# Performance work log

Hardware: AMD Instinct MI355X
Metric: run time of the kernel (lower is better)

The kernel has to match this reference:

```python
import jax, jax.numpy as jnp
import numpy as np

LAYERS, HIDDEN, FFN, HEADS = 2, 128, 256, 4
IMG_H, IMG_W = 32, 64
SEQ = IMG_H * IMG_W
HEAD = HIDDEN // HEADS          # 32, per-head qk dim
HEAD_V = 2 * HEAD               # double_v_dim=True
VDIM = HEADS * HEAD_V           # 256
B = 2
SCALE_BASE = 512.0
EPS = 1e-5


def _xpos_tables(seq, d):
    # XPOS: rotary angles + per-position exponential scale
    half = d // 2
    scale_vec = (jnp.arange(0, d, 2, dtype=jnp.float32) + 0.4 * d) / (1.4 * d)  # (d/2,)
    power = jnp.arange(seq, dtype=jnp.float32) / SCALE_BASE
    scale = scale_vec[None, :] ** power[:, None]                                 # (S, d/2)
    inv_freq = 1.0 / (10000.0 ** (jnp.arange(half, dtype=jnp.float32) / half))
    ang = jnp.arange(seq, dtype=jnp.float32)[:, None] * inv_freq[None, :]        # (S, d/2)
    return jnp.sin(ang), jnp.cos(ang), scale


def _apply_xpos(x, sin, cos, scale):
    # duplicate-interleave sin/cos*scale to width d, rotate-every-two
    s = jnp.repeat(sin * scale, 2, axis=-1)   # (S, d)
    c = jnp.repeat(cos * scale, 2, axis=-1)
    x1, x2 = x[..., ::2], x[..., 1::2]
    rot = jnp.stack([-x2, x1], axis=-1).reshape(x.shape)
    return x * c + rot * s


def _ln(x, g, b):
    mu = x.mean(-1, keepdims=True)
    var = ((x - mu) ** 2).mean(-1, keepdims=True)
    return (x - mu) * jax.lax.rsqrt(var + EPS) * g + b


def _gn(y, g, b):
    # GroupNorm(HEADS groups) over VDIM channels, applied per token
    bsz, s, v = y.shape
    yg = y.reshape(bsz, s, HEADS, HEAD_V)
    mu = yg.mean(-1, keepdims=True)
    var = ((yg - mu) ** 2).mean(-1, keepdims=True)
    yn = ((yg - mu) * jax.lax.rsqrt(var + EPS)).reshape(bsz, s, v)
    return yn * g + b


def _decay(seq):
    # D[h, n, m] = gamma_h^(n-m) for n >= m else 0
    gammas = 1.0 - jnp.exp(jnp.linspace(jnp.log(1.0 / 32.0), jnp.log(1.0 / 512.0), HEADS))
    n = jnp.arange(seq, dtype=jnp.float32)
    diff = n[:, None] - n[None, :]
    return (gammas[:, None, None] ** jnp.maximum(diff, 0.0)) * (diff >= 0.0)


def _forward(x, ln1_g, ln1_b, ln2_g, ln2_b, WQ, WK, WV, WG, WO, gn_g, gn_b, w1, b1, w2, b2):
    sin, cos, scale = _xpos_tables(SEQ, HEAD)
    D = _decay(SEQ)  # (H, S, S)
    for i in range(LAYERS):
        h = _ln(x, ln1_g[i], ln1_b[i])
        Q = _apply_xpos(jnp.einsum('bsd,hde->bhse', h, WQ[i]), sin, cos, scale)
        K = _apply_xpos(jnp.einsum('bsd,hde->bhse', h, WK[i]), sin, cos, 1.0 / scale)
        V = jnp.einsum('bsd,hdv->bhsv', h, WV[i])
        att = jnp.einsum('bhse,bhte->bhst', Q, K) * D[None]      # decay retention
        Y = jnp.einsum('bhst,bhtv->bhsv', att, V)
        Y = jnp.moveaxis(Y, 1, 2).reshape(x.shape[0], SEQ, VDIM)  # concat heads
        Y = _gn(Y, gn_g[i], gn_b[i])
        G = h @ WG[i]
        ret = (G * jax.nn.sigmoid(G) * Y) @ WO[i]                 # swish gate + out proj
        y = ret + x
        h2 = _ln(y, ln2_g[i], ln2_b[i])
        x = jax.nn.gelu(h2 @ w1[i] + b1[i], approximate=False) @ w2[i] + b2[i] + y
    return x.reshape(x.shape[0], IMG_H, IMG_W, x.shape[-1])


def setup_inputs() -> dict:
    key = jax.random.key(0)
    ks = jax.random.split(key, 8)
    def rn(k, shape, sc):
        return jax.random.normal(k, shape, dtype=jnp.float32) * sc
    s = 1.0 / np.sqrt(HIDDEN)
    return {
        'x': rn(ks[0], (B, SEQ, HIDDEN), 1.0),
        'ln1_g': jnp.ones((LAYERS, HIDDEN), jnp.float32),
        'ln1_b': jnp.zeros((LAYERS, HIDDEN), jnp.float32),
        'ln2_g': jnp.ones((LAYERS, HIDDEN), jnp.float32),
        'ln2_b': jnp.zeros((LAYERS, HIDDEN), jnp.float32),
        'WQ': rn(ks[1], (LAYERS, HEADS, HIDDEN, HEAD), s),
        'WK': rn(ks[2], (LAYERS, HEADS, HIDDEN, HEAD), s),
        'WV': rn(ks[3], (LAYERS, HEADS, HIDDEN, HEAD_V), s),
        'WG': rn(ks[4], (LAYERS, HIDDEN, VDIM), s),
        'WO': rn(ks[5], (LAYERS, VDIM, HIDDEN), 1.0 / np.sqrt(VDIM)),
        'gn_g': jnp.ones((LAYERS, VDIM), jnp.float32),
        'gn_b': jnp.zeros((LAYERS, VDIM), jnp.float32),
        'w1': rn(ks[6], (LAYERS, HIDDEN, FFN), s),
        'b1': jnp.zeros((LAYERS, FFN), jnp.float32),
        'w2': rn(ks[7], (LAYERS, FFN, HIDDEN), 1.0 / np.sqrt(FFN)),
        'b2': jnp.zeros((LAYERS, HIDDEN), jnp.float32),
    }


def reference(x, ln1_g, ln1_b, ln2_g, ln2_b, WQ, WK, WV, WG, WO, gn_g, gn_b, w1, b1, w2, b2):
    return _forward(x, ln1_g, ln1_b, ln2_g, ln2_b, WQ, WK, WV, WG, WO, gn_g, gn_b, w1, b1, w2, b2)
```

## Files before the change

kernel.cpp:

```cpp
#include <hip/hip_runtime.h>
#include <math.h>

#define NLAYERS 2
#define HID 128
#define FFND 256
#define NH 4
#define SEQL 2048
#define HD 32
#define HDV 64
#define VD 256
#define NBATCH 2
#define MROWS (NBATCH*SEQL)
#define NCAT 768
#define NCHUNK 32

__global__ __launch_bounds__(256) void setup_kernel(
    const float* __restrict__ WQ, const float* __restrict__ WK,
    const float* __restrict__ WV, const float* __restrict__ WG,
    float* __restrict__ Wcat, float* __restrict__ tabs)
{
  int bid = blockIdx.x;
  if (bid < 768) {
    int idx = bid * 256 + threadIdx.x;
    int l = idx / (HID * NCAT);
    int r = idx - l * (HID * NCAT);
    int k = r / NCAT;
    int n = r - k * NCAT;
    float v;
    if (n < 128)      { int h = n >> 5, e = n & 31;            v = WQ[(((l*NH+h)*HID)+k)*HD  + e]; }
    else if (n < 256) { int m = n-128; int h = m>>5, e = m&31; v = WK[(((l*NH+h)*HID)+k)*HD  + e]; }
    else if (n < 512) { int m = n-256; int h = m>>6, e = m&63; v = WV[(((l*NH+h)*HID)+k)*HDV + e]; }
    else              { v = WG[(l*HID + k)*VD + (n-512)]; }
    Wcat[idx] = v;
  } else {
    int idx = (bid - 768) * 256 + threadIdx.x;
    int s = idx >> 4, i = idx & 15;
    float inv_freq = powf(10000.f, -(float)i * (1.f/16.f));
    float ang = (float)s * inv_freq;
    float sv  = ((float)(2*i) + 0.4f*32.f) / (1.4f*32.f);
    float sc  = powf(sv, (float)s * (1.f/512.f));
    float sn = sinf(ang), cs = cosf(ang);
    tabs[idx]          = sn * sc;
    tabs[32768 + idx]  = cs * sc;
    tabs[65536 + idx]  = sn / sc;
    tabs[98304 + idx]  = cs / sc;
  }
}

template<int CN, bool XPOS, bool BIAS, bool GELU>
__global__ __launch_bounds__(256) void gemm_ln(
    const float* __restrict__ A, const float* __restrict__ Bw,
    const float* __restrict__ lng, const float* __restrict__ lnb,
    const float* __restrict__ bias, const float* __restrict__ tabs,
    float* __restrict__ C, int N)
{
  constexpr int TN = 16 * CN;
  constexpr int BK = (CN == 8) ? 32 : 64;
  __shared__ float As[128][68];
  __shared__ float Bs[BK][TN + 4];

  int tid = threadIdx.x;
  int tx = tid & 15, ty = tid >> 4;
  int rb = blockIdx.x * 64, nb = blockIdx.y * TN;

  {
    int row = tid >> 2, q = tid & 3;
    const float* ar = A + (size_t)(rb + row) * HID + 32 * q;
    float4 av[8];
    #pragma unroll
    for (int it = 0; it < 8; it++) av[it] = *(const float4*)(ar + 4*it);
    float s = 0.f;
    #pragma unroll
    for (int it = 0; it < 8; it++) s += av[it].x + av[it].y + av[it].z + av[it].w;
    s += __shfl_xor(s, 1); s += __shfl_xor(s, 2);
    float mu = s * (1.f/128.f);
    float qs = 0.f;
    #pragma unroll
    for (int it = 0; it < 8; it++) {
      float d;
      d = av[it].x - mu; qs += d*d;  d = av[it].y - mu; qs += d*d;
      d = av[it].z - mu; qs += d*d;  d = av[it].w - mu; qs += d*d;
    }
    qs += __shfl_xor(qs, 1); qs += __shfl_xor(qs, 2);
    float rs = rsqrtf(qs * (1.f/128.f) + 1e-5f);
    int rsw = row ^ (16 * q);
    #pragma unroll
    for (int it = 0; it < 8; it++) {
      int k0 = 32*q + 4*it;
      float4 g4 = *(const float4*)(lng + k0);
      float4 b4 = *(const float4*)(lnb + k0);
      As[k0+0][rsw] = (av[it].x-mu)*rs*g4.x + b4.x;
      As[k0+1][rsw] = (av[it].y-mu)*rs*g4.y + b4.y;
      As[k0+2][rsw] = (av[it].z-mu)*rs*g4.z + b4.z;
      As[k0+3][rsw] = (av[it].w-mu)*rs*g4.w + b4.w;
    }
  }

  float acc[4][CN];
  #pragma unroll
  for (int i=0;i<4;i++)
    #pragma unroll
    for (int j=0;j<CN;j++) acc[i][j] = 0.f;

  for (int ks = 0; ks < 128; ks += BK) {
    #pragma unroll
    for (int it = 0; it < 4; it++) {
      int idx = it*256 + tid;
      int kk = idx / (TN/4), nq = idx % (TN/4);
      *(float4*)(&Bs[kk][4*nq]) =
          *(const float4*)(Bw + (size_t)(ks+kk)*N + nb + 4*nq);
    }
    __syncthreads();
    #pragma unroll
    for (int kk = 0; kk < BK; kk++) {
      int k = ks + kk;
      float a[4];
      *(float4*)a = *(const float4*)&As[k][(4*ty) ^ (16*(k>>5))];
      float b[CN];
      #pragma unroll
      for (int j4 = 0; j4 < CN; j4 += 4)
        *(float4*)(b+j4) = *(const float4*)&Bs[kk][CN*tx + j4];
      #pragma unroll
      for (int i=0;i<4;i++)
        #pragma unroll
        for (int j=0;j<CN;j++)
          acc[i][j] = fmaf(a[i], b[j], acc[i][j]);
    }
    __syncthreads();
  }

  #pragma unroll
  for (int i=0;i<4;i++) {
    int row = rb + 4*ty + i;
    int cb = nb + CN*tx;
    float o[CN];
    #pragma unroll
    for (int j=0;j<CN;j++) {
      float v = acc[i][j];
      if (BIAS)  v += bias[cb + j];
      if (GELU)  v = 0.5f * v * (1.f + erff(v * 0.70710678118f));
      o[j] = v;
    }
    if (XPOS) {
      if (nb < 256) {
        bool isK = (nb >= 128);
        const float* sn_t = tabs + (isK ? 65536 : 0);
        const float* cs_t = tabs + (isK ? 98304 : 32768);
        int s = row & (SEQL - 1);
        #pragma unroll
        for (int p = 0; p < CN/2; p++) {
          int i0 = ((cb + 2*p) & 31) >> 1;
          float sn = sn_t[s*16 + i0], cs = cs_t[s*16 + i0];
          float x1 = o[2*p], x2 = o[2*p+1];
          o[2*p]   = x1*cs - x2*sn;
          o[2*p+1] = x2*cs + x1*sn;
        }
      }
    }
    #pragma unroll
    for (int j4 = 0; j4 < CN; j4 += 4)
      *(float4*)(C + (size_t)row*N + cb + j4) = *(float4*)(o + j4);
  }
}

template<bool BIAS>
__global__ __launch_bounds__(256) void gemm_nar(
    const float* __restrict__ A, const float* __restrict__ Bw,
    const float* __restrict__ bias, const float* __restrict__ Rsd,
    float* __restrict__ C, int N)
{
  __shared__ float As[64][68];
  __shared__ float Bs[64][36];
  int tid = threadIdx.x;
  int tx = tid & 15, ty = tid >> 4;
  int rb = blockIdx.x * 64, nb = blockIdx.y * 32;

  float acc[4][2];
  #pragma unroll
  for (int i=0;i<4;i++) { acc[i][0]=0.f; acc[i][1]=0.f; }

  for (int ks = 0; ks < 256; ks += 64) {
    #pragma unroll
    for (int it = 0; it < 4; it++) {
      int idx = it*256 + tid;
      int row = idx >> 4, kq = idx & 15;
      float4 a4 = *(const float4*)(A + (size_t)(rb+row)*256 + ks + 4*kq);
      int rsw = row ^ (4*(kq & 7));
      As[4*kq+0][rsw] = a4.x; As[4*kq+1][rsw] = a4.y;
      As[4*kq+2][rsw] = a4.z; As[4*kq+3][rsw] = a4.w;
    }
    #pragma unroll
    for (int it = 0; it < 2; it++) {
      int idx = it*256 + tid;
      int kk = idx >> 3, nq = idx & 7;
      *(float4*)(&Bs[kk][4*nq]) =
          *(const float4*)(Bw + (size_t)(ks+kk)*N + nb + 4*nq);
    }
    __syncthreads();
    #pragma unroll
    for (int kk = 0; kk < 64; kk++) {
      float a[4];
      *(float4*)a = *(const float4*)&As[kk][(4*ty) ^ (4*((kk>>2)&7))];
      float2 b2 = *(const float2*)&Bs[kk][2*tx];
      #pragma unroll
      for (int i=0;i<4;i++) {
        acc[i][0] = fmaf(a[i], b2.x, acc[i][0]);
        acc[i][1] = fmaf(a[i], b2.y, acc[i][1]);
      }
    }
    __syncthreads();
  }

  #pragma unroll
  for (int i=0;i<4;i++) {
    int row = rb + 4*ty + i;
    int cb = nb + 2*tx;
    float o[2];
    #pragma unroll
    for (int j=0;j<2;j++) {
      float v = acc[i][j];
      if (BIAS) v += bias[cb + j];
      v += Rsd[(size_t)row*N + cb + j];
      o[j] = v;
    }
    *(float2*)(C + (size_t)row*N + cb) = *(float2*)o;
  }
}

__global__ __launch_bounds__(512) void ret_kv_kernel(
    const float* __restrict__ QKVG, float* __restrict__ Asum)
{
  int bh = blockIdx.x >> 5;
  int c  = blockIdx.x & 31;
  int b = bh >> 2, h = bh & 3;
  float t0 = logf(1.f/32.f) + (float)h * (logf(1.f/512.f) - logf(1.f/32.f)) * (1.f/3.f);
  float gamma = 1.f - expf(t0);
  float lg = logf(gamma);

  __shared__ float Ks[64][36];
  __shared__ float Vs[64][68];
  __shared__ float wt[64];

  int tid = threadIdx.x;
  int c0 = c * 64;
  const float* base = QKVG + (size_t)(b * SEQL) * NCAT;

  {
    int row = tid >> 3, eq = tid & 7;
    *(float4*)&Ks[row][4*eq] =
        *(const float4*)(base + (size_t)(c0+row)*NCAT + 128 + h*32 + 4*eq);
  }
  #pragma unroll
  for (int it = 0; it < 2; it++) {
    int idx = it*512 + tid;
    int row = idx >> 4, vq = idx & 15;
    *(float4*)&Vs[row][4*vq] =
        *(const float4*)(base + (size_t)(c0+row)*NCAT + 256 + h*64 + 4*vq);
  }
  if (tid < 64) wt[tid] = __expf(lg * (float)(64 - tid));
  __syncthreads();

  int e = tid >> 4, v4 = (tid & 15) * 4;
  float a0[4] = {0,0,0,0};
  #pragma unroll 8
  for (int t = 0; t < 64; t++) {
    float kw = Ks[t][e] * wt[t];
    float4 v0 = *(const float4*)&Vs[t][v4];
    a0[0] = fmaf(kw, v0.x, a0[0]); a0[1] = fmaf(kw, v0.y, a0[1]);
    a0[2] = fmaf(kw, v0.z, a0[2]); a0[3] = fmaf(kw, v0.w, a0[3]);
  }
  *(float4*)(Asum + ((size_t)(bh*NCHUNK + c))*2048 + e*64 + v4) = *(float4*)a0;
}

__global__ __launch_bounds__(512) void ret_out_kernel(
    const float* __restrict__ QKVG, const float* __restrict__ Asum,
    const float* __restrict__ gn_g, const float* __restrict__ gn_b,
    float* __restrict__ Gated)
{
  int bh = blockIdx.x >> 5;
  int c  = blockIdx.x & 31;
  int b = bh >> 2, h = bh & 3;
  float t0 = logf(1.f/32.f) + (float)h * (logf(1.f/512.f) - logf(1.f/32.f)) * (1.f/3.f);
  float gamma = 1.f - expf(t0);
  float lg = logf(gamma);
  float g64 = __expf(lg * 64.f);

  __shared__ float Qs[64][36];
  __shared__ float Ks[64][36];
  __shared__ float Vs[64][68];
  __shared__ float Ss[64][68];
  __shared__ float Sc[32][68];

  int tid = threadIdx.x;
  int tx2 = tid & 31, ty2 = tid >> 5;
  int c0 = c * 64;
  const float* base = QKVG + (size_t)(b * SEQL) * NCAT;

  {
    int row = tid >> 3, eq = tid & 7;
    *(float4*)&Qs[row][4*eq] =
        *(const float4*)(base + (size_t)(c0+row)*NCAT + h*32 + 4*eq);
    int esw = (4*eq) ^ (4*((row >> 2) & 7));
    *(float4*)&Ks[row][esw] =
        *(const float4*)(base + (size_t)(c0+row)*NCAT + 128 + h*32 + 4*eq);
  }
  #pragma unroll
  for (int it = 0; it < 2; it++) {
    int idx = it*512 + tid;
    int row = idx >> 4, vq = idx & 15;
    *(float4*)&Vs[row][4*vq] =
        *(const float4*)(base + (size_t)(c0+row)*NCAT + 256 + h*64 + 4*vq);
  }

  {
    int e = tid >> 4, v4 = (tid & 15) * 4;
    float s0[4] = {0,0,0,0};
    float w = 1.f;
    const float* ab = Asum + ((size_t)bh*NCHUNK)*2048 + e*64 + v4;
    for (int cp = c-1; cp >= 0; --cp) {
      const float* ap = ab + (size_t)cp*2048;
      float4 x0 = *(const float4*)ap;
      s0[0] = fmaf(w, x0.x, s0[0]); s0[1] = fmaf(w, x0.y, s0[1]);
      s0[2] = fmaf(w, x0.z, s0[2]); s0[3] = fmaf(w, x0.w, s0[3]);
      w *= g64;
    }
    *(float4*)&Sc[e][v4] = *(float4*)s0;
  }
  __syncthreads();

  float sacc[4][2];
  #pragma unroll
  for (int i=0;i<4;i++) { sacc[i][0]=0.f; sacc[i][1]=0.f; }
  #pragma unroll
  for (int e = 0; e < 32; e += 4) {
    float qv[4][4], kv[2][4];
    #pragma unroll
    for (int i=0;i<4;i++)
      *(float4*)qv[i] = *(const float4*)&Qs[4*ty2+i][e];
    #pragma unroll
    for (int j=0;j<2;j++) {
      int kr = 2*tx2 + j;
      *(float4*)kv[j] = *(const float4*)&Ks[kr][e ^ (4*((kr>>2)&7))];
    }
    #pragma unroll
    for (int i=0;i<4;i++)
      #pragma unroll
      for (int j=0;j<2;j++)
        sacc[i][j] = fmaf(qv[i][0], kv[j][0],
                     fmaf(qv[i][1], kv[j][1],
                     fmaf(qv[i][2], kv[j][2],
                     fmaf(qv[i][3], kv[j][3], sacc[i][j]))));
  }
  #pragma unroll
  for (int i=0;i<4;i++) {
    int sl = 4*ty2 + i;
    float o2[2];
    #pragma unroll
    for (int j=0;j<2;j++) {
      int dr = sl - (2*tx2 + j);
      float w = (dr >= 0) ? __expf(lg * (float)dr) : 0.f;
      o2[j] = sacc[i][j] * w;
    }
    *(float2*)&Ss[sl][2*tx2] = *(float2*)o2;
  }

  float acc[4][2];
  #pragma unroll
  for (int i=0;i<4;i++) { acc[i][0]=0.f; acc[i][1]=0.f; }
  #pragma unroll
  for (int e = 0; e < 32; e += 4) {
    float qv[4][4], sv[4][2];
    #pragma unroll
    for (int i=0;i<4;i++)
      *(float4*)qv[i] = *(const float4*)&Qs[4*ty2+i][e];
    #pragma unroll
    for (int m=0;m<4;m++)
      *(float2*)sv[m] = *(const float2*)&Sc[e+m][2*tx2];
    #pragma unroll
    for (int i=0;i<4;i++)
      #pragma unroll
      for (int j=0;j<2;j++)
        acc[i][j] = fmaf(qv[i][0], sv[0][j],
                    fmaf(qv[i][1], sv[1][j],
                    fmaf(qv[i][2], sv[2][j],
                    fmaf(qv[i][3], sv[3][j], acc[i][j]))));
  }
  #pragma unroll
  for (int i=0;i<4;i++) {
    float gr = __expf(lg * (float)(4*ty2 + i));
    acc[i][0] *= gr; acc[i][1] *= gr;
  }
  __syncthreads();

  #pragma unroll
  for (int t = 0; t < 64; t += 4) {
    float sv[4][4], vv[4][2];
    #pragma unroll
    for (int i=0;i<4;i++)
      *(float4*)sv[i] = *(const float4*)&Ss[4*ty2+i][t];
    #pragma unroll
    for (int m=0;m<4;m++)
      *(float2*)vv[m] = *(const float2*)&Vs[t+m][2*tx2];
    #pragma unroll
    for (int i=0;i<4;i++)
      #pragma unroll
      for (int j=0;j<2;j++)
        acc[i][j] = fmaf(sv[i][0], vv[0][j],
                    fmaf(sv[i][1], vv[1][j],
                    fmaf(sv[i][2], vv[2][j],
                    fmaf(sv[i][3], vv[3][j], acc[i][j]))));
  }

  #pragma unroll
  for (int i=0;i<4;i++) {
    float s1 = acc[i][0] + acc[i][1];
    #pragma unroll
    for (int o = 16; o; o >>= 1) s1 += __shfl_xor(s1, o);
    float mu = s1 * (1.f/64.f);
    float q = 0.f;
    #pragma unroll
    for (int j=0;j<2;j++) { float d = acc[i][j] - mu; q += d*d; }
    #pragma unroll
    for (int o = 16; o; o >>= 1) q += __shfl_xor(q, o);
    float rs = rsqrtf(q * (1.f/64.f) + 1e-5f);
    int row = b*SEQL + c0 + 4*ty2 + i;
    float2 g2 = *(const float2*)(QKVG + (size_t)row*NCAT + 512 + h*64 + 2*tx2);
    float gv[2] = {g2.x, g2.y};
    float o2[2];
    #pragma unroll
    for (int j=0;j<2;j++) {
      int col = h*64 + 2*tx2 + j;
      float yn = (acc[i][j] - mu) * rs * gn_g[col] + gn_b[col];
      float g = gv[j];
      float sig = 1.f / (1.f + __expf(-g));
      o2[j] = g * sig * yn;
    }
    *(float2*)(Gated + (size_t)row*VD + h*64 + 2*tx2) = *(float2*)o2;
  }
}

extern "C" void kernel_launch(void* const* d_in, const int* in_sizes, int n_in,
                              void* d_out, int out_size, void* d_ws, size_t ws_size,
                              hipStream_t stream)
{
  (void)in_sizes; (void)n_in; (void)out_size; (void)ws_size;
  const float* x_in  = (const float*)d_in[0];
  const float* ln1_g = (const float*)d_in[1];
  const float* ln1_b = (const float*)d_in[2];
  const float* ln2_g = (const float*)d_in[3];
  const float* ln2_b = (const float*)d_in[4];
  const float* WQ    = (const float*)d_in[5];
  const float* WK    = (const float*)d_in[6];
  const float* WV    = (const float*)d_in[7];
  const float* WG    = (const float*)d_in[8];
  const float* WO    = (const float*)d_in[9];
  const float* gn_g  = (const float*)d_in[10];
  const float* gn_b  = (const float*)d_in[11];
  const float* w1    = (const float*)d_in[12];
  const float* b1    = (const float*)d_in[13];
  const float* w2    = (const float*)d_in[14];
  const float* b2    = (const float*)d_in[15];
  float* out = (float*)d_out;
  float* ws  = (float*)d_ws;

  float* Wcat = ws;
  float* tabs = Wcat + 196608;
  float* QKVG = tabs + 131072;
  float* Asum = QKVG + 3145728;
  float* Gt   = Asum + 524288;
  float* Yres = Gt   + 1048576;
  float* Mid  = Yres + 524288;

  setup_kernel<<<896, 256, 0, stream>>>(WQ, WK, WV, WG, Wcat, tabs);

  for (int l = 0; l < NLAYERS; l++) {
    const float* xl = (l == 0) ? x_in : out;
    gemm_ln<8,true,false,false><<<dim3(MROWS/64, NCAT/128), 256, 0, stream>>>(
        xl, Wcat + l*HID*NCAT, ln1_g + l*HID, ln1_b + l*HID,
        nullptr, tabs, QKVG, NCAT);
    ret_kv_kernel<<<256, 512, 0, stream>>>(QKVG, Asum);
    ret_out_kernel<<<256, 512, 0, stream>>>(QKVG, Asum, gn_g + l*VD, gn_b + l*VD, Gt);
    gemm_nar<false><<<dim3(MROWS/64, HID/32), 256, 0, stream>>>(
        Gt, WO + l*VD*HID, nullptr, xl, Yres, HID);
    gemm_ln<4,false,true,true><<<dim3(MROWS/64, FFND/64), 256, 0, stream>>>(
        Yres, w1 + l*HID*FFND, ln2_g + l*HID, ln2_b + l*HID,
        b1 + l*FFND, nullptr, Mid, FFND);
    gemm_nar<true><<<dim3(MROWS/64, HID/32), 256, 0, stream>>>(
        Mid, w2 + l*FFND*HID, b2 + l*HID, Yres, out, HID);
  }
}
```

Measured before the change: 236.5 us.

## Fuse output projection, LayerNorm and FFN into one chained kernel

Replaces the three separate post-retention GEMM launches (WO plus residual, LN2+FFN1+GELU, FFN2 plus residual) with one ffn_chain kernel. It keeps each 16-row tile's intermediates in shared memory, so Yres and Mid no longer round-trip through global memory. The QKVG projection is split into a standalone LayerNorm kernel plus a new register-prefetched GEMM that computes the XPOS sin/cos/scale inline, which removes the precomputed tables. In exchange, each fused block re-streams all FFN weights for only 16 rows, and the projection epilogue now evaluates transcendentals per element.

```diff
diff --git a/kernel.cpp b/kernel.cpp
--- a/kernel.cpp
+++ b/kernel.cpp
@@ -14,216 +14,140 @@
 #define NCAT 768
 #define NCHUNK 32
 
-__global__ __launch_bounds__(256) void setup_kernel(
+#define LG32   (-3.4657359028f)
+#define DLT    (-0.9241962407f)
+__device__ __forceinline__ float lgamma_h(int h) {
+  return logf(1.f - expf(LG32 + DLT * (float)h));
+}
+
+__global__ __launch_bounds__(256) void pack_w_kernel(
     const float* __restrict__ WQ, const float* __restrict__ WK,
     const float* __restrict__ WV, const float* __restrict__ WG,
-    float* __restrict__ Wcat, float* __restrict__ tabs)
+    float* __restrict__ Wcat)
 {
-  int bid = blockIdx.x;
-  if (bid < 768) {
-    int idx = bid * 256 + threadIdx.x;
-    int l = idx / (HID * NCAT);
-    int r = idx - l * (HID * NCAT);
-    int k = r / NCAT;
-    int n = r - k * NCAT;
-    float v;
-    if (n < 128)      { int h = n >> 5, e = n & 31;            v = WQ[(((l*NH+h)*HID)+k)*HD  + e]; }
-    else if (n < 256) { int m = n-128; int h = m>>5, e = m&31; v = WK[(((l*NH+h)*HID)+k)*HD  + e]; }
-    else if (n < 512) { int m = n-256; int h = m>>6, e = m&63; v = WV[(((l*NH+h)*HID)+k)*HDV + e]; }
-    else              { v = WG[(l*HID + k)*VD + (n-512)]; }
-    Wcat[idx] = v;
-  } else {
-    int idx = (bid - 768) * 256 + threadIdx.x;
-    int s = idx >> 4, i = idx & 15;
-    float inv_freq = powf(10000.f, -(float)i * (1.f/16.f));
-    float ang = (float)s * inv_freq;
-    float sv  = ((float)(2*i) + 0.4f*32.f) / (1.4f*32.f);
-    float sc  = powf(sv, (float)s * (1.f/512.f));
-    float sn = sinf(ang), cs = cosf(ang);
-    tabs[idx]          = sn * sc;
-    tabs[32768 + idx]  = cs * sc;
-    tabs[65536 + idx]  = sn / sc;
-    tabs[98304 + idx]  = cs / sc;
-  }
-}
-
-template<int CN, bool XPOS, bool BIAS, bool GELU>
-__global__ __launch_bounds__(256) void gemm_ln(
-    const float* __restrict__ A, const float* __restrict__ Bw,
-    const float* __restrict__ lng, const float* __restrict__ lnb,
-    const float* __restrict__ bias, const float* __restrict__ tabs,
-    float* __restrict__ C, int N)
+  int idx = blockIdx.x * 256 + threadIdx.x;
+  if (idx >= NLAYERS * HID * NCAT) return;
+  int l = idx / (HID * NCAT);
+  int r = idx - l * (HID * NCAT);
+  int k = r / NCAT;
+  int n = r - k * NCAT;
+  float v;
+  if (n < 128)      { int h = n >> 5, e = n & 31;            v = WQ[(((l*NH+h)*HID)+k)*HD  + e]; }
+  else if (n < 256) { int m = n-128; int h = m>>5, e = m&31; v = WK[(((l*NH+h)*HID)+k)*HD  + e]; }
+  else if (n < 512) { int m = n-256; int h = m>>6, e = m&63; v = WV[(((l*NH+h)*HID)+k)*HDV + e]; }
+  else              { v = WG[(l*HID + k)*VD + (n-512)]; }
+  Wcat[idx] = v;
+}
+
+__global__ __launch_bounds__(256) void ln_rows_kernel(
+    const float* __restrict__ X, const float* __restrict__ g,
+    const float* __restrict__ b, float* __restrict__ O)
 {
-  constexpr int TN = 16 * CN;
-  constexpr int BK = (CN == 8) ? 32 : 64;
-  __shared__ float As[128][68];
-  __shared__ float Bs[BK][TN + 4];
-
+  int wid = threadIdx.x >> 6, lane = threadIdx.x & 63;
+  int row = blockIdx.x * 4 + wid;
+  const float* x = X + (size_t)row * HID;
+  float v0 = x[lane], v1 = x[lane + 64];
+  float s = v0 + v1;
+  #pragma unroll
+  for (int o = 32; o; o >>= 1) s += __shfl_xor(s, o);
+  float mu = s * (1.f/128.f);
+  float d0 = v0 - mu, d1 = v1 - mu;
+  float q = d0*d0 + d1*d1;
+  #pragma unroll
+  for (int o = 32; o; o >>= 1) q += __shfl_xor(q, o);
+  float rs = rsqrtf(q * (1.f/128.f) + 1e-5f);
+  O[(size_t)row*HID + lane]      = d0 * rs * g[lane]      + b[lane];
+  O[(size_t)row*HID + lane + 64] = d1 * rs * g[lane + 64] + b[lane + 64];
+}
+
+__global__ __launch_bounds__(512) void gemm_qkvg(
+    const float* __restrict__ H, const float* __restrict__ Wcat,
+    float* __restrict__ C)
+{
+  __shared__ float Bs[16][260];
   int tid = threadIdx.x;
-  int tx = tid & 15, ty = tid >> 4;
-  int rb = blockIdx.x * 64, nb = blockIdx.y * TN;
-
-  {
-    int row = tid >> 2, q = tid & 3;
-    const float* ar = A + (size_t)(rb + row) * HID + 32 * q;
-    float4 av[8];
-    #pragma unroll
-    for (int it = 0; it < 8; it++) av[it] = *(const float4*)(ar + 4*it);
-    float s = 0.f;
-    #pragma unroll
-    for (int it = 0; it < 8; it++) s += av[it].x + av[it].y + av[it].z + av[it].w;
-    s += __shfl_xor(s, 1); s += __shfl_xor(s, 2);
-    float mu = s * (1.f/128.f);
-    float qs = 0.f;
-    #pragma unroll
-    for (int it = 0; it < 8; it++) {
-      float d;
-      d = av[it].x - mu; qs += d*d;  d = av[it].y - mu; qs += d*d;
-      d = av[it].z - mu; qs += d*d;  d = av[it].w - mu; qs += d*d;
-    }
-    qs += __shfl_xor(qs, 1); qs += __shfl_xor(qs, 2);
-    float rs = rsqrtf(qs * (1.f/128.f) + 1e-5f);
-    int rsw = row ^ (16 * q);
-    #pragma unroll
-    for (int it = 0; it < 8; it++) {
-      int k0 = 32*q + 4*it;
-      float4 g4 = *(const float4*)(lng + k0);
-      float4 b4 = *(const float4*)(lnb + k0);
-      As[k0+0][rsw] = (av[it].x-mu)*rs*g4.x + b4.x;
-      As[k0+1][rsw] = (av[it].y-mu)*rs*g4.y + b4.y;
-      As[k0+2][rsw] = (av[it].z-mu)*rs*g4.z + b4.z;
-      As[k0+3][rsw] = (av[it].w-mu)*rs*g4.w + b4.w;
-    }
-  }
-
-  float acc[4][CN];
+  int tx = tid & 63, ty = tid >> 6;
+  int rb = blockIdx.x * 32, nb = blockIdx.y * 256;
+
+  float4 pre[2];
+  #pragma unroll
+  for (int it = 0; it < 2; it++) {
+    int f = it*512 + tid;
+    int kk = f >> 6, c4 = f & 63;
+    pre[it] = *(const float4*)(Wcat + (size_t)kk*NCAT + nb + 4*c4);
+  }
+
+  float acc[4][4];
   #pragma unroll
   for (int i=0;i<4;i++)
     #pragma unroll
-    for (int j=0;j<CN;j++) acc[i][j] = 0.f;
-
-  for (int ks = 0; ks < 128; ks += BK) {
-    #pragma unroll
-    for (int it = 0; it < 4; it++) {
-      int idx = it*256 + tid;
-      int kk = idx / (TN/4), nq = idx % (TN/4);
-      *(float4*)(&Bs[kk][4*nq]) =
-          *(const float4*)(Bw + (size_t)(ks+kk)*N + nb + 4*nq);
+    for (int j=0;j<4;j++) acc[i][j] = 0.f;
+
+  for (int kt = 0; kt < 8; kt++) {
+    int ks = kt * 16;
+    #pragma unroll
+    for (int it = 0; it < 2; it++) {
+      int f = it*512 + tid;
+      int kk = f >> 6, c4 = f & 63;
+      *(float4*)&Bs[kk][4*c4] = pre[it];
     }
     __syncthreads();
-    #pragma unroll
-    for (int kk = 0; kk < BK; kk++) {
-      int k = ks + kk;
-      float a[4];
-      *(float4*)a = *(const float4*)&As[k][(4*ty) ^ (16*(k>>5))];
-      float b[CN];
-      #pragma unroll
-      for (int j4 = 0; j4 < CN; j4 += 4)
-        *(float4*)(b+j4) = *(const float4*)&Bs[kk][CN*tx + j4];
+    if (kt + 1 < 8) {
+      #pragma unroll
+      for (int it = 0; it < 2; it++) {
+        int f = it*512 + tid;
+        int kk = f >> 6, c4 = f & 63;
+        pre[it] = *(const float4*)(Wcat + (size_t)(ks+16+kk)*NCAT + nb + 4*c4);
+      }
+    }
+    #pragma unroll
+    for (int k0 = 0; k0 < 16; k0 += 4) {
+      float4 av[4];
       #pragma unroll
       for (int i=0;i<4;i++)
-        #pragma unroll
-        for (int j=0;j<CN;j++)
-          acc[i][j] = fmaf(a[i], b[j], acc[i][j]);
+        av[i] = *(const float4*)(H + (size_t)(rb + 4*ty + i)*HID + ks + k0);
+      float4 bv[4];
+      #pragma unroll
+      for (int kq=0;kq<4;kq++)
+        bv[kq] = *(const float4*)&Bs[k0+kq][4*tx];
+      #pragma unroll
+      for (int i=0;i<4;i++) {
+        float a4[4] = {av[i].x, av[i].y, av[i].z, av[i].w};
+        #pragma unroll
+        for (int kq=0;kq<4;kq++) {
+          acc[i][0] = fmaf(a4[kq], bv[kq].x, acc[i][0]);
+          acc[i][1] = fmaf(a4[kq], bv[kq].y, acc[i][1]);
+          acc[i][2] = fmaf(a4[kq], bv[kq].z, acc[i][2]);
+          acc[i][3] = fmaf(a4[kq], bv[kq].w, acc[i][3]);
+        }
+      }
     }
     __syncthreads();
   }
 
+  int col0 = nb + 4*tx;
   #pragma unroll
   for (int i=0;i<4;i++) {
     int row = rb + 4*ty + i;
-    int cb = nb + CN*tx;
-    float o[CN];
-    #pragma unroll
-    for (int j=0;j<CN;j++) {
-      float v = acc[i][j];
-      if (BIAS)  v += bias[cb + j];
-      if (GELU)  v = 0.5f * v * (1.f + erff(v * 0.70710678118f));
-      o[j] = v;
-    }
-    if (XPOS) {
-      if (nb < 256) {
-        bool isK = (nb >= 128);
-        const float* sn_t = tabs + (isK ? 65536 : 0);
-        const float* cs_t = tabs + (isK ? 98304 : 32768);
-        int s = row & (SEQL - 1);
-        #pragma unroll
-        for (int p = 0; p < CN/2; p++) {
-          int i0 = ((cb + 2*p) & 31) >> 1;
-          float sn = sn_t[s*16 + i0], cs = cs_t[s*16 + i0];
-          float x1 = o[2*p], x2 = o[2*p+1];
-          o[2*p]   = x1*cs - x2*sn;
-          o[2*p+1] = x2*cs + x1*sn;
-        }
-      }
-    }
-    #pragma unroll
-    for (int j4 = 0; j4 < CN; j4 += 4)
-      *(float4*)(C + (size_t)row*N + cb + j4) = *(float4*)(o + j4);
-  }
-}
-
-template<bool BIAS>
-__global__ __launch_bounds__(256) void gemm_nar(
-    const float* __restrict__ A, const float* __restrict__ Bw,
-    const float* __restrict__ bias, const float* __restrict__ Rsd,
-    float* __restrict__ C, int N)
-{
-  __shared__ float As[64][68];
-  __shared__ float Bs[64][36];
-  int tid = threadIdx.x;
-  int tx = tid & 15, ty = tid >> 4;
-  int rb = blockIdx.x * 64, nb = blockIdx.y * 32;
-
-  float acc[4][2];
-  #pragma unroll
-  for (int i=0;i<4;i++) { acc[i][0]=0.f; acc[i][1]=0.f; }
-
-  for (int ks = 0; ks < 256; ks += 64) {
-    #pragma unroll
-    for (int it = 0; it < 4; it++) {
-      int idx = it*256 + tid;
-      int row = idx >> 4, kq = idx & 15;
-      float4 a4 = *(const float4*)(A + (size_t)(rb+row)*256 + ks + 4*kq);
-      int rsw = row ^ (4*(kq & 7));
-      As[4*kq+0][rsw] = a4.x; As[4*kq+1][rsw] = a4.y;
-      As[4*kq+2][rsw] = a4.z; As[4*kq+3][rsw] = a4.w;
-    }
-    #pragma unroll
-    for (int it = 0; it < 2; it++) {
-      int idx = it*256 + tid;
-      int kk = idx >> 3, nq = idx & 7;
-      *(float4*)(&Bs[kk][4*nq]) =
-          *(const float4*)(Bw + (size_t)(ks+kk)*N + nb + 4*nq);
-    }
-    __syncthreads();
-    #pragma unroll
-    for (int kk = 0; kk < 64; kk++) {
-      float a[4];
-      *(float4*)a = *(const float4*)&As[kk][(4*ty) ^ (4*((kk>>2)&7))];
-      float2 b2 = *(const float2*)&Bs[kk][2*tx];
-      #pragma unroll
-      for (int i=0;i<4;i++) {
-        acc[i][0] = fmaf(a[i], b2.x, acc[i][0]);
-        acc[i][1] = fmaf(a[i], b2.y, acc[i][1]);
-      }
-    }
-    __syncthreads();
-  }
-
-  #pragma unroll
-  for (int i=0;i<4;i++) {
-    int row = rb + 4*ty + i;
-    int cb = nb + 2*tx;
-    float o[2];
-    #pragma unroll
-    for (int j=0;j<2;j++) {
-      float v = acc[i][j];
-      if (BIAS) v += bias[cb + j];
-      v += Rsd[(size_t)row*N + cb + j];
-      o[j] = v;
-    }
-    *(float2*)(C + (size_t)row*N + cb) = *(float2*)o;
+    float o[4] = {acc[i][0], acc[i][1], acc[i][2], acc[i][3]};
+    if (col0 < 256) {
+      bool isK = (col0 >= 128);
+      float sgn = isK ? -1.f : 1.f;
+      float s = (float)(row & (SEQL - 1));
+      #pragma unroll
+      for (int p = 0; p < 2; p++) {
+        float fi   = (float)(((col0 & 31) >> 1) + p);
+        float invf = exp2f(fi * -0.83048202372f);
+        float sv   = (2.f*fi + 12.8f) * (1.f/44.8f);
+        float sc   = exp2f(log2f(sv) * (1.f/512.f) * sgn * s);
+        float ang  = s * invf;
+        float sn = sinf(ang) * sc, cs = cosf(ang) * sc;
+        float x1 = o[2*p], x2 = o[2*p+1];
+        o[2*p]   = x1*cs - x2*sn;
+        o[2*p+1] = x2*cs + x1*sn;
+      }
+    }
+    *(float4*)(C + (size_t)row*NCAT + col0) = *(float4*)o;
   }
 }
 
@@ -233,9 +157,7 @@
   int bh = blockIdx.x >> 5;
   int c  = blockIdx.x & 31;
   int b = bh >> 2, h = bh & 3;
-  float t0 = logf(1.f/32.f) + (float)h * (logf(1.f/512.f) - logf(1.f/32.f)) * (1.f/3.f);
-  float gamma = 1.f - expf(t0);
-  float lg = logf(gamma);
+  float lg = lgamma_h(h);
 
   __shared__ float Ks[64][36];
   __shared__ float Vs[64][68];
@@ -280,9 +202,7 @@
   int bh = blockIdx.x >> 5;
   int c  = blockIdx.x & 31;
   int b = bh >> 2, h = bh & 3;
-  float t0 = logf(1.f/32.f) + (float)h * (logf(1.f/512.f) - logf(1.f/32.f)) * (1.f/3.f);
-  float gamma = 1.f - expf(t0);
-  float lg = logf(gamma);
+  float lg = lgamma_h(h);
   float g64 = __expf(lg * 64.f);
 
   __shared__ float Qs[64][36];
@@ -436,6 +356,222 @@
       o2[j] = g * sig * yn;
     }
     *(float2*)(Gated + (size_t)row*VD + h*64 + 2*tx2) = *(float2*)o2;
+  }
+}
+
+__global__ __launch_bounds__(512) void ffn_chain(
+    const float* __restrict__ Gated, const float* __restrict__ WO,
+    const float* __restrict__ Xres,
+    const float* __restrict__ lng, const float* __restrict__ lnb,
+    const float* __restrict__ w1, const float* __restrict__ b1,
+    const float* __restrict__ w2, const float* __restrict__ b2,
+    float* __restrict__ Out)
+{
+  __shared__ float WsBuf[32*132];
+  __shared__ float h2s[16][132];
+  __shared__ float Ms[16][260];
+
+  int tid = threadIdx.x;
+  int rb = blockIdx.x * 16;
+  int tx = tid & 63, ty = tid >> 6;
+
+  float yr[2][2];
+  {
+    float4 pre[2];
+    #pragma unroll
+    for (int it = 0; it < 2; it++) {
+      int f = it*512 + tid;
+      int kk = f >> 5, c4 = f & 31;
+      pre[it] = *(const float4*)(WO + (size_t)kk*HID + 4*c4);
+    }
+    float acc[2][2] = {{0.f,0.f},{0.f,0.f}};
+    for (int kt = 0; kt < 8; kt++) {
+      int ks = kt * 32;
+      #pragma unroll
+      for (int it = 0; it < 2; it++) {
+        int f = it*512 + tid;
+        int kk = f >> 5, c4 = f & 31;
+        *(float4*)&WsBuf[kk*132 + 4*c4] = pre[it];
+      }
+      __syncthreads();
+      if (kt + 1 < 8) {
+        #pragma unroll
+        for (int it = 0; it < 2; it++) {
+          int f = it*512 + tid;
+          int kk = f >> 5, c4 = f & 31;
+          pre[it] = *(const float4*)(WO + (size_t)(ks+32+kk)*HID + 4*c4);
+        }
+      }
+      #pragma unroll
+      for (int k0 = 0; k0 < 32; k0 += 4) {
+        float4 av[2];
+        #pragma unroll
+        for (int i=0;i<2;i++)
+          av[i] = *(const float4*)(Gated + (size_t)(rb + 2*ty + i)*VD + ks + k0);
+        float2 bv[4];
+        #pragma unroll
+        for (int kq=0;kq<4;kq++)
+          bv[kq] = *(const float2*)&WsBuf[(k0+kq)*132 + 2*tx];
+        #pragma unroll
+        for (int i=0;i<2;i++) {
+          float a4[4] = {av[i].x, av[i].y, av[i].z, av[i].w};
+          #pragma unroll
+          for (int kq=0;kq<4;kq++) {
+            acc[i][0] = fmaf(a4[kq], bv[kq].x, acc[i][0]);
+            acc[i][1] = fmaf(a4[kq], bv[kq].y, acc[i][1]);
+          }
+        }
+      }
+      __syncthreads();
+    }
+    #pragma unroll
+    for (int i=0;i<2;i++) {
+      float2 xr = *(const float2*)(Xres + (size_t)(rb + 2*ty + i)*HID + 2*tx);
+      yr[i][0] = acc[i][0] + xr.x;
+      yr[i][1] = acc[i][1] + xr.y;
+    }
+  }
+
+  #pragma unroll
+  for (int i=0;i<2;i++) {
+    float s = yr[i][0] + yr[i][1];
+    #pragma unroll
+    for (int o = 32; o; o >>= 1) s += __shfl_xor(s, o);
+    float mu = s * (1.f/128.f);
+    float d0 = yr[i][0]-mu, d1 = yr[i][1]-mu;
+    float q = d0*d0 + d1*d1;
+    #pragma unroll
+    for (int o = 32; o; o >>= 1) q += __shfl_xor(q, o);
+    float rs = rsqrtf(q * (1.f/128.f) + 1e-5f);
+    float o2[2] = { d0*rs*lng[2*tx+0] + lnb[2*tx+0],
+                    d1*rs*lng[2*tx+1] + lnb[2*tx+1] };
+    *(float2*)&h2s[2*ty+i][2*tx] = *(float2*)o2;
+  }
+  __syncthreads();
+
+  {
+    float4 pre[2];
+    #pragma unroll
+    for (int it = 0; it < 2; it++) {
+      int f = it*512 + tid;
+      int kk = f >> 6, c4 = f & 63;
+      pre[it] = *(const float4*)(w1 + (size_t)kk*FFND + 4*c4);
+    }
+    float acc[2][4];
+    #pragma unroll
+    for (int i=0;i<2;i++)
+      #pragma unroll
+      for (int j=0;j<4;j++) acc[i][j] = 0.f;
+    for (int kt = 0; kt < 8; kt++) {
+      int ks = kt * 16;
+      #pragma unroll
+      for (int it = 0; it < 2; it++) {
+        int f = it*512 + tid;
+        int kk = f >> 6, c4 = f & 63;
+        *(float4*)&WsBuf[kk*260 + 4*c4] = pre[it];
+      }
+      __syncthreads();
+      if (kt + 1 < 8) {
+        #pragma unroll
+        for (int it = 0; it < 2; it++) {
+          int f = it*512 + tid;
+          int kk = f >> 6, c4 = f & 63;
+          pre[it] = *(const float4*)(w1 + (size_t)(ks+16+kk)*FFND + 4*c4);
+        }
+      }
+      #pragma unroll
+      for (int k0 = 0; k0 < 16; k0 += 4) {
+        float4 av[2];
+        #pragma unroll
+        for (int i=0;i<2;i++)
+          av[i] = *(const float4*)&h2s[2*ty+i][ks + k0];
+        float4 bv[4];
+        #pragma unroll
+        for (int kq=0;kq<4;kq++)
+          bv[kq] = *(const float4*)&WsBuf[(k0+kq)*260 + 4*tx];
+        #pragma unroll
+        for (int i=0;i<2;i++) {
+          float a4[4] = {av[i].x, av[i].y, av[i].z, av[i].w};
+          #pragma unroll
+          for (int kq=0;kq<4;kq++) {
+            acc[i][0] = fmaf(a4[kq], bv[kq].x, acc[i][0]);
+            acc[i][1] = fmaf(a4[kq], bv[kq].y, acc[i][1]);
+            acc[i][2] = fmaf(a4[kq], bv[kq].z, acc[i][2]);
+            acc[i][3] = fmaf(a4[kq], bv[kq].w, acc[i][3]);
+          }
+        }
+      }
+      __syncthreads();
+    }
+    float4 bi = *(const float4*)(b1 + 4*tx);
+    float bvi[4] = {bi.x, bi.y, bi.z, bi.w};
+    #pragma unroll
+    for (int i=0;i<2;i++) {
+      float o[4];
+      #pragma unroll
+      for (int j=0;j<4;j++) {
+        float v = acc[i][j] + bvi[j];
+        o[j] = 0.5f * v * (1.f + erff(v * 0.70710678118f));
+      }
+      *(float4*)&Ms[2*ty+i][4*tx] = *(float4*)o;
+    }
+  }
+  __syncthreads();
+
+  {
+    float4 pre[2];
+    #pragma unroll
+    for (int it = 0; it < 2; it++) {
+      int f = it*512 + tid;
+      int kk = f >> 5, c4 = f & 31;
+      pre[it] = *(const float4*)(w2 + (size_t)kk*HID + 4*c4);
+    }
+    float acc[2][2] = {{0.f,0.f},{0.f,0.f}};
+    for (int kt = 0; kt < 8; kt++) {
+      int ks = kt * 32;
+      #pragma unroll
+      for (int it = 0; it < 2; it++) {
+        int f = it*512 + tid;
+        int kk = f >> 5, c4 = f & 31;
+        *(float4*)&WsBuf[kk*132 + 4*c4] = pre[it];
+      }
+      __syncthreads();
+      if (kt + 1 < 8) {
+        #pragma unroll
+        for (int it = 0; it < 2; it++) {
+          int f = it*512 + tid;
+          int kk = f >> 5, c4 = f & 31;
+          pre[it] = *(const float4*)(w2 + (size_t)(ks+32+kk)*HID + 4*c4);
+        }
+      }
+      #pragma unroll
+      for (int k0 = 0; k0 < 32; k0 += 4) {
+        float4 av[2];
+        #pragma unroll
+        for (int i=0;i<2;i++)
+          av[i] = *(const float4*)&Ms[2*ty+i][ks + k0];
+        float2 bv[4];
+        #pragma unroll
+        for (int kq=0;kq<4;kq++)
+          bv[kq] = *(const float2*)&WsBuf[(k0+kq)*132 + 2*tx];
+        #pragma unroll
+        for (int i=0;i<2;i++) {
+          float a4[4] = {av[i].x, av[i].y, av[i].z, av[i].w};
+          #pragma unroll
+          for (int kq=0;kq<4;kq++) {
+            acc[i][0] = fmaf(a4[kq], bv[kq].x, acc[i][0]);
+            acc[i][1] = fmaf(a4[kq], bv[kq].y, acc[i][1]);
+          }
+        }
+      }
+      __syncthreads();
+    }
+    #pragma unroll
+    for (int i=0;i<2;i++) {
+      float o2[2] = { acc[i][0] + b2[2*tx+0] + yr[i][0],
+                      acc[i][1] + b2[2*tx+1] + yr[i][1] };
+      *(float2*)(Out + (size_t)(rb + 2*ty + i)*HID + 2*tx) = *(float2*)o2;
+    }
   }
 }
 
@@ -464,28 +600,21 @@
   float* ws  = (float*)d_ws;
 
   float* Wcat = ws;
-  float* tabs = Wcat + 196608;
-  float* QKVG = tabs + 131072;
+  float* Hbuf = Wcat + 196608;
+  float* QKVG = Hbuf + 524288;
   float* Asum = QKVG + 3145728;
   float* Gt   = Asum + 524288;
-  float* Yres = Gt   + 1048576;
-  float* Mid  = Yres + 524288;
-
-  setup_kernel<<<896, 256, 0, stream>>>(WQ, WK, WV, WG, Wcat, tabs);
+
+  pack_w_kernel<<<768, 256, 0, stream>>>(WQ, WK, WV, WG, Wcat);
 
   for (int l = 0; l < NLAYERS; l++) {
     const float* xl = (l == 0) ? x_in : out;
-    gemm_ln<8,true,false,false><<<dim3(MROWS/64, NCAT/128), 256, 0, stream>>>(
-        xl, Wcat + l*HID*NCAT, ln1_g + l*HID, ln1_b + l*HID,
-        nullptr, tabs, QKVG, NCAT);
+    ln_rows_kernel<<<MROWS/4, 256, 0, stream>>>(xl, ln1_g + l*HID, ln1_b + l*HID, Hbuf);
+    gemm_qkvg<<<dim3(MROWS/32, 3), 512, 0, stream>>>(Hbuf, Wcat + l*HID*NCAT, QKVG);
     ret_kv_kernel<<<256, 512, 0, stream>>>(QKVG, Asum);
     ret_out_kernel<<<256, 512, 0, stream>>>(QKVG, Asum, gn_g + l*VD, gn_b + l*VD, Gt);
-    gemm_nar<false><<<dim3(MROWS/64, HID/32), 256, 0, stream>>>(
-        Gt, WO + l*VD*HID, nullptr, xl, Yres, HID);
-    gemm_ln<4,false,true,true><<<dim3(MROWS/64, FFND/64), 256, 0, stream>>>(
-        Yres, w1 + l*HID*FFND, ln2_g + l*HID, ln2_b + l*HID,
-        b1 + l*FFND, nullptr, Mid, FFND);
-    gemm_nar<true><<<dim3(MROWS/64, HID/32), 256, 0, stream>>>(
-        Mid, w2 + l*FFND*HID, b2 + l*HID, Yres, out, HID);
-  }
-}
+    ffn_chain<<<256, 512, 0, stream>>>(
+        Gt, WO + l*VD*HID, xl, ln2_g + l*HID, ln2_b + l*HID,
+        w1 + l*HID*FFND, b1 + l*FFND, w2 + l*FFND*HID, b2 + l*HID, out);
+  }
+}
```

After: 329.3 us. 39.2% more time.
